# Kernel optimization log

Hardware: AMD Instinct MI355X
Metric: run time of the kernel (lower is better)

## Reference

```python
import jax, jax.numpy as jnp
import numpy as np

B = 32768                 # batch size (number of variants)
NUM_READ_FEATURES = 11
NUM_INFO_FEATURES = 9
PHI_DIMS = [NUM_READ_FEATURES, 64, 64]
OMEGA_DIMS = [NUM_INFO_FEATURES, 64, 64]
RHO_DIMS = [2 * 64 + 64, 128, 64, 1]
CAL_DIMS = [2, 5, 5, 1]


def _counts():
    # deterministic ragged group sizes in [5, 32], mean ~18.5, all nonempty
    return 5 + (np.arange(2 * B) % 28)


def _mlp_params(key, dims, prefix, out):
    for i, (din, dout) in enumerate(zip(dims[:-1], dims[1:])):
        key, k = jax.random.split(key)
        out[f"{prefix}_w{i}"] = (jax.random.normal(k, (din, dout), jnp.float32)
                                  / np.sqrt(din).astype(np.float32))
        out[f"{prefix}_b{i}"] = jnp.zeros((dout,), jnp.float32)
    return key


def _mlp(x, ws_bs):
    # Linear -> ReLU between layers, no activation after the last layer
    n = len(ws_bs) // 2
    for i in range(n):
        x = x @ ws_bs[2 * i] + ws_bs[2 * i + 1]
        if i < n - 1:
            x = jax.nn.relu(x)
    return x


def setup_inputs() -> dict:
    key = jax.random.key(0)
    counts = _counts()
    n_reads = int(counts.sum())  # 1,212,320
    key, k1, k2 = jax.random.split(key, 3)
    out = {
        "reads": jax.random.normal(k1, (n_reads, NUM_READ_FEATURES), jnp.float32),
        "info": jax.random.normal(k2, (B, NUM_INFO_FEATURES), jnp.float32),
        "end_indices": jnp.asarray(np.cumsum(counts), dtype=jnp.int64),
    }
    key = _mlp_params(key, PHI_DIMS, "phi", out)
    key = _mlp_params(key, OMEGA_DIMS, "omega", out)
    key = _mlp_params(key, RHO_DIMS, "rho", out)
    key = _mlp_params(key, CAL_DIMS, "cal", out)
    out["max_logit"] = jnp.asarray(10.0, jnp.float32)
    return out


def reference(reads, info, end_indices,
              phi_w0, phi_b0, phi_w1, phi_b1,
              omega_w0, omega_b0, omega_w1, omega_b1,
              rho_w0, rho_b0, rho_w1, rho_b1, rho_w2, rho_b2,
              cal_w0, cal_b0, cal_w1, cal_b1, cal_w2, cal_b2,
              max_logit):
    n_reads = reads.shape[0]
    num_seg = 2 * B
    # read r belongs to segment j where end_indices[j-1] <= r < end_indices[j]
    seg_ids = jnp.searchsorted(end_indices, jnp.arange(n_reads), side="right")

    phi_reads = jax.nn.sigmoid(_mlp(reads, [phi_w0, phi_b0, phi_w1, phi_b1]))  # [N, 64]
    weights = jnp.ones((n_reads, 1), phi_reads.dtype)  # weight_range == 0
    weighted = weights * phi_reads

    read_sums = jax.ops.segment_sum(weighted, seg_ids, num_segments=num_seg)      # [2B, 64]
    weight_sums = jax.ops.segment_sum(weights, seg_ids, num_segments=num_seg)     # [2B, 1]
    read_means = read_sums / weight_sums
    sq_weight_sums = jax.ops.segment_sum(jnp.square(weights), seg_ids, num_segments=num_seg)
    eff_counts = jnp.square(weight_sums) / sq_weight_sums                          # [2B, 1]

    ref_means, alt_means = read_means[:B], read_means[B:]
    eff_ref, eff_alt = eff_counts[:B], eff_counts[B:]

    omega_info = jax.nn.sigmoid(_mlp(info, [omega_w0, omega_b0, omega_w1, omega_b1]))
    concatenated = jnp.concatenate([ref_means, alt_means, omega_info], axis=1)     # [B, 192]
    logits = jnp.squeeze(_mlp(concatenated, [rho_w0, rho_b0, rho_w1, rho_b1, rho_w2, rho_b2]), -1)

    # Calibration: temperature from sqrt(alt_count), sqrt(ref_count)
    sqrt_counts = jnp.concatenate([jnp.sqrt(eff_alt), jnp.sqrt(eff_ref)], axis=1)  # [B, 2]
    temperatures = jnp.squeeze(_mlp(sqrt_counts, [cal_w0, cal_b0, cal_w1, cal_b1, cal_w2, cal_b2]), -1)
    calibrated = logits * temperatures
    return max_logit * jnp.tanh(calibrated / max_logit)
```

## Files before the change

### kernel.cpp

```cpp
#include <hip/hip_runtime.h>
#include <hip/hip_bf16.h>
#include <math.h>

#define NB 32768
#define NSEG 65536
#define NRF 11
#define NIF 9

typedef __attribute__((ext_vector_type(8))) short bf16x8;
typedef __attribute__((ext_vector_type(4))) float f32x4;

__device__ __forceinline__ short to_bf(float f) {
    __hip_bfloat16 h = __float2bfloat16(f);
    return *reinterpret_cast<short*>(&h);
}
__device__ __forceinline__ float bf2f(short s) {
    __hip_bfloat16 h = *reinterpret_cast<__hip_bfloat16*>(&s);
    return __bfloat162float(h);
}

__global__ __launch_bounds__(256) void k0_prep(
    const float* __restrict__ rw0, const float* __restrict__ rw1,
    const float* __restrict__ pw0, const float* __restrict__ pw1,
    short* __restrict__ w0th, short* __restrict__ w0tl,
    short* __restrict__ w1th, short* __restrict__ w1tl,
    short* __restrict__ p_w0t, short* __restrict__ p_w1t)
{
    const int idx = blockIdx.x * 256 + threadIdx.x;
    if (idx < 192 * 128) {
        const int k = idx >> 7, col = idx & 127;
        const float v = rw0[idx];
        const short hi = to_bf(v);
        const short lo = to_bf(v - bf2f(hi));
        w0th[col * 192 + k] = hi;
        w0tl[col * 192 + k] = lo;
    }
    if (idx < 128 * 64) {
        const int k = idx >> 6, col = idx & 63;
        const float v = rw1[idx];
        const short hi = to_bf(v);
        const short lo = to_bf(v - bf2f(hi));
        w1th[col * 128 + k] = hi;
        w1tl[col * 128 + k] = lo;
    }
    if (idx < 64 * 16) {
        const int col = idx >> 4, k = idx & 15;
        p_w0t[idx] = (k < NRF) ? to_bf(pw0[k * 64 + col]) : (short)0;
    }
    if (idx < 64 * 64) {
        const int col = idx >> 6, k = idx & 63;
        p_w1t[idx] = to_bf(pw1[k * 64 + col]);
    }
}

__global__ __launch_bounds__(256, 4) void k1_phi_mfma6(
    const float* __restrict__ reads,
    const int* __restrict__ endi,
    const short* __restrict__ p_w0t, const short* __restrict__ p_w1t,
    const float* __restrict__ b0, const float* __restrict__ b1,
    float* __restrict__ means)
{
    __shared__ short XA[256][24];
    __shared__ short HB[4][16][64];
    __shared__ int   smeta[9];

    const int tid  = threadIdx.x;
    const int lane = tid & 63;
    const int w    = tid >> 6;
    const int lg   = lane >> 4;
    const int lr   = lane & 15;
    const int k0   = lg * 8;
    const int s0   = blockIdx.x * 8;

    if (tid < 9) {
        const int s = s0 + tid - 1;
        smeta[tid] = (s < 0) ? 0 : endi[s];
    }
    __syncthreads();
    const int rb    = smeta[0];
    const int nrows = smeta[8] - rb;

    const int total = nrows * NRF;
    const float* __restrict__ rbase = reads + (size_t)rb * NRF;
    for (int i = tid; i < total; i += 256) {
        const int row = i / NRF;
        const int col = i - row * NRF;
        XA[row][col] = to_bf(rbase[i]);
    }
    for (int r = tid; r < nrows; r += 256) {
        XA[r][11] = 0;
        *(short4*)&XA[r][12] = (short4){0, 0, 0, 0};
    }
    __syncthreads();

    bf16x8 aW0[4];
#pragma unroll
    for (int nt = 0; nt < 4; ++nt) {
        bf16x8 z = {0, 0, 0, 0, 0, 0, 0, 0};
        if (lg < 2) z = *(const bf16x8*)&p_w0t[(nt * 16 + lr) * 16 + k0];
        aW0[nt] = z;
    }
    bf16x8 bW1[4][2];
#pragma unroll
    for (int nt = 0; nt < 4; ++nt)
#pragma unroll
        for (int ks = 0; ks < 2; ++ks)
            bW1[nt][ks] = *(const bf16x8*)&p_w1t[(nt * 16 + lr) * 64 + ks * 32 + k0];

    f32x4 cbias0[4];
#pragma unroll
    for (int nt = 0; nt < 4; ++nt)
#pragma unroll
        for (int q = 0; q < 4; ++q) cbias0[nt][q] = b0[nt * 16 + 4 * lg + q];
    f32x4 cbias1[4];
#pragma unroll
    for (int nt = 0; nt < 4; ++nt) {
        const float bv = b1[nt * 16 + lr];
#pragma unroll
        for (int q = 0; q < 4; ++q) cbias1[nt][q] = bv;
    }

    for (int q = 0; q < 2; ++q) {
        const int ls  = q * 4 + w;
        const int st  = smeta[ls] - rb;
        const int cnt = smeta[ls + 1] - smeta[ls];
        const int ntl = (cnt + 15) >> 4;
        float segsum[4] = {0.f, 0.f, 0.f, 0.f};

        for (int tt = 0; tt < ntl; ++tt) {
            int lrow = st + tt * 16 + lr;
            lrow = (lrow < nrows) ? lrow : (nrows - 1);
            bf16x8 xb = {0, 0, 0, 0, 0, 0, 0, 0};
            if (lg < 2) xb = *(const bf16x8*)&XA[lrow][k0];

            f32x4 d[4];
#pragma unroll
            for (int nt = 0; nt < 4; ++nt)
                d[nt] = __builtin_amdgcn_mfma_f32_16x16x32_bf16(aW0[nt], xb, cbias0[nt], 0, 0, 0);

#pragma unroll
            for (int nt = 0; nt < 4; ++nt) {
                short4 hp;
                hp.x = to_bf(fmaxf(d[nt][0], 0.f));
                hp.y = to_bf(fmaxf(d[nt][1], 0.f));
                hp.z = to_bf(fmaxf(d[nt][2], 0.f));
                hp.w = to_bf(fmaxf(d[nt][3], 0.f));
                const int blk = (2 * nt + (lg >> 1) + lr) & 7;
                *(short4*)&HB[w][lr][(blk << 3) + ((lg & 1) << 2)] = hp;
            }
            const bf16x8 h0 = *(const bf16x8*)&HB[w][lr][(((lg + lr) & 7) << 3)];
            const bf16x8 h1 = *(const bf16x8*)&HB[w][lr][(((4 + lg + lr) & 7) << 3)];
            f32x4 o[4];
#pragma unroll
            for (int nt = 0; nt < 4; ++nt) {
                f32x4 t = __builtin_amdgcn_mfma_f32_16x16x32_bf16(h0, bW1[nt][0], cbias1[nt], 0, 0, 0);
                o[nt]   = __builtin_amdgcn_mfma_f32_16x16x32_bf16(h1, bW1[nt][1], t, 0, 0, 0);
            }
            const int rowg = tt * 16 + 4 * lg;
#pragma unroll
            for (int nt = 0; nt < 4; ++nt) {
                float s = 0.f;
#pragma unroll
                for (int q2 = 0; q2 < 4; ++q2) {
                    const float p = __builtin_amdgcn_rcpf(1.f + __expf(-o[nt][q2]));
                    s += (rowg + q2 < cnt) ? p : 0.f;
                }
                segsum[nt] += s;
            }
        }
#pragma unroll
        for (int nt = 0; nt < 4; ++nt) {
            segsum[nt] += __shfl_xor(segsum[nt], 16);
            segsum[nt] += __shfl_xor(segsum[nt], 32);
        }
        if (lg == 0) {
            const float inv = 1.f / (float)cnt;
#pragma unroll
            for (int nt = 0; nt < 4; ++nt)
                means[(size_t)(s0 + ls) * 64 + nt * 16 + lr] = segsum[nt] * inv;
        }
    }
}

__global__ __launch_bounds__(256) void k2_omega(
    const float* __restrict__ info,
    const float* __restrict__ w0, const float* __restrict__ b0,
    const float* __restrict__ w1, const float* __restrict__ b1,
    float* __restrict__ om)
{
    __shared__ float hbuf[4][64];
    const int lane = threadIdx.x & 63;
    const int wid  = threadIdx.x >> 6;
    const int wg   = __builtin_amdgcn_readfirstlane((int)(blockIdx.x * 4 + wid));

    float w0c[NIF];
#pragma unroll
    for (int k = 0; k < NIF; ++k) w0c[k] = w0[k * 64 + lane];
    float w1c[64];
#pragma unroll
    for (int i = 0; i < 64; ++i) w1c[i] = w1[i * 64 + lane];
    const float b0l = b0[lane];
    const float b1l = b1[lane];

    for (int i = 0; i < 8; ++i) {
        const int b = wg * 8 + i;
        const float* __restrict__ x = info + (size_t)b * NIF;
        float h = b0l;
#pragma unroll
        for (int k = 0; k < NIF; ++k) h = fmaf(x[k], w0c[k], h);
        h = fmaxf(h, 0.f);
        hbuf[wid][lane] = h;
        float o = b1l;
        const float4* h4 = (const float4*)(&hbuf[wid][0]);
#pragma unroll
        for (int q = 0; q < 16; ++q) {
            float4 hv = h4[q];
            o = fmaf(hv.x, w1c[4 * q + 0], o);
            o = fmaf(hv.y, w1c[4 * q + 1], o);
            o = fmaf(hv.z, w1c[4 * q + 2], o);
            o = fmaf(hv.w, w1c[4 * q + 3], o);
        }
        om[(size_t)b * 64 + lane] = 1.f / (1.f + __expf(-o));
    }
}

__global__ __launch_bounds__(256) void k3_rho_mfma(
    const float* __restrict__ means, const float* __restrict__ om,
    const int* __restrict__ endi,
    const short* __restrict__ w0th, const short* __restrict__ w0tl,
    const short* __restrict__ w1th, const short* __restrict__ w1tl,
    const float* __restrict__ rb0, const float* __restrict__ rb1,
    const float* __restrict__ rw2, const float* __restrict__ rb2,
    const float* __restrict__ cw0, const float* __restrict__ cb0,
    const float* __restrict__ cw1, const float* __restrict__ cb1,
    const float* __restrict__ cw2, const float* __restrict__ cb2,
    const float* __restrict__ max_logit,
    float* __restrict__ out)
{
    __shared__ __align__(16) char smemA[18432];
    __shared__ __align__(16) char smemB[34816];
    short (*XH)[72]  = (short(*)[72])smemA;
    short (*XL)[72]  = (short(*)[72])(smemA + 9216);
    short (*HH)[136] = (short(*)[136])smemB;
    short (*HL)[136] = (short(*)[136])(smemB + 17408);
    float (*h2T)[68] = (float(*)[68])smemA;

    const int tid  = threadIdx.x;
    const int lane = tid & 63;
    const int w    = tid >> 6;
    const int lg   = lane >> 4;
    const int lr   = lane & 15;
    const int k0   = lg * 8;
    const int b0i  = blockIdx.x * 64;

    const int wbase = w * 32;
    float bias0[2];
#pragma unroll
    for (int nt = 0; nt < 2; ++nt) bias0[nt] = rb0[wbase + nt * 16 + lr];

    f32x4 acc[4][2];
#pragma unroll
    for (int rt = 0; rt < 4; ++rt)
#pragma unroll
        for (int nt = 0; nt < 2; ++nt) acc[rt][nt] = (f32x4){0.f, 0.f, 0.f, 0.f};

    for (int c = 0; c < 3; ++c) {
        const float* __restrict__ src =
            (c == 0) ? means + (size_t)b0i * 64 :
            (c == 1) ? means + (size_t)(NB + b0i) * 64 :
                       om    + (size_t)b0i * 64;
        __syncthreads();
        for (int idx = tid; idx < 64 * 64; idx += 256) {
            const int row = idx >> 6, col = idx & 63;
            const float v = src[(size_t)row * 64 + col];
            const short hi = to_bf(v);
            const short lo = to_bf(v - bf2f(hi));
            XH[row][col] = hi;
            XL[row][col] = lo;
        }
        __syncthreads();

#pragma unroll
        for (int ks = 0; ks < 2; ++ks) {
            const int koff = c * 64 + ks * 32 + k0;
            bf16x8 Bh[2], Bl[2];
#pragma unroll
            for (int nt = 0; nt < 2; ++nt) {
                const int col = wbase + nt * 16 + lr;
                Bh[nt] = *(const bf16x8*)&w0th[(size_t)col * 192 + koff];
                Bl[nt] = *(const bf16x8*)&w0tl[(size_t)col * 192 + koff];
            }
#pragma unroll
            for (int rt = 0; rt < 4; ++rt) {
                const bf16x8 Ah = *(const bf16x8*)&XH[rt * 16 + lr][ks * 32 + k0];
                const bf16x8 Al = *(const bf16x8*)&XL[rt * 16 + lr][ks * 32 + k0];
#pragma unroll
                for (int nt = 0; nt < 2; ++nt) {
                    acc[rt][nt] = __builtin_amdgcn_mfma_f32_16x16x32_bf16(Ah, Bh[nt], acc[rt][nt], 0, 0, 0);
                    acc[rt][nt] = __builtin_amdgcn_mfma_f32_16x16x32_bf16(Al, Bh[nt], acc[rt][nt], 0, 0, 0);
                    acc[rt][nt] = __builtin_amdgcn_mfma_f32_16x16x32_bf16(Ah, Bl[nt], acc[rt][nt], 0, 0, 0);
                }
            }
        }
    }
    __syncthreads();
#pragma unroll
    for (int rt = 0; rt < 4; ++rt)
#pragma unroll
        for (int nt = 0; nt < 2; ++nt)
#pragma unroll
            for (int r = 0; r < 4; ++r) {
                const int row = rt * 16 + 4 * lg + r;
                const int col = wbase + nt * 16 + lr;
                const float v = fmaxf(acc[rt][nt][r] + bias0[nt], 0.f);
                const short hi = to_bf(v);
                HH[row][col] = hi;
                HL[row][col] = to_bf(v - bf2f(hi));
            }
    __syncthreads();

    const int cbase = w * 16;
    const float bias1 = rb1[cbase + lr];
    f32x4 acc2[4];
#pragma unroll
    for (int rt = 0; rt < 4; ++rt) acc2[rt] = (f32x4){0.f, 0.f, 0.f, 0.f};

#pragma unroll
    for (int ks = 0; ks < 4; ++ks) {
        const int koff = ks * 32 + k0;
        const int col  = cbase + lr;
        const bf16x8 Bh = *(const bf16x8*)&w1th[(size_t)col * 128 + koff];
        const bf16x8 Bl = *(const bf16x8*)&w1tl[(size_t)col * 128 + koff];
#pragma unroll
        for (int rt = 0; rt < 4; ++rt) {
            const bf16x8 Ah = *(const bf16x8*)&HH[rt * 16 + lr][koff];
            const bf16x8 Al = *(const bf16x8*)&HL[rt * 16 + lr][koff];
            acc2[rt] = __builtin_amdgcn_mfma_f32_16x16x32_bf16(Ah, Bh, acc2[rt], 0, 0, 0);
            acc2[rt] = __builtin_amdgcn_mfma_f32_16x16x32_bf16(Al, Bh, acc2[rt], 0, 0, 0);
            acc2[rt] = __builtin_amdgcn_mfma_f32_16x16x32_bf16(Ah, Bl, acc2[rt], 0, 0, 0);
        }
    }
#pragma unroll
    for (int rt = 0; rt < 4; ++rt)
#pragma unroll
        for (int r = 0; r < 4; ++r)
            h2T[cbase + lr][rt * 16 + 4 * lg + r] = fmaxf(acc2[rt][r] + bias1, 0.f);
    __syncthreads();

    if (w == 0) {
        const int b = b0i + lane;
        float l0 = rb2[0], l1 = 0.f, l2 = 0.f, l3 = 0.f;
#pragma unroll
        for (int j = 0; j < 16; ++j) {
            l0 = fmaf(h2T[j][lane],      rw2[j],      l0);
            l1 = fmaf(h2T[16 + j][lane], rw2[16 + j], l1);
            l2 = fmaf(h2T[32 + j][lane], rw2[32 + j], l2);
            l3 = fmaf(h2T[48 + j][lane], rw2[48 + j], l3);
        }
        const float logit = (l0 + l1) + (l2 + l3);

        const int er1 = endi[b];
        const int er0 = (b == 0) ? 0 : endi[b - 1];
        const int ea1 = endi[NB + b];
        const int ea0 = endi[NB + b - 1];
        const float x0 = sqrtf((float)(ea1 - ea0));
        const float x1 = sqrtf((float)(er1 - er0));

        float t5[5];
#pragma unroll
        for (int m = 0; m < 5; ++m)
            t5[m] = fmaxf(cb0[m] + x0 * cw0[m] + x1 * cw0[5 + m], 0.f);
        float t5b[5];
#pragma unroll
        for (int m = 0; m < 5; ++m) {
            float v = cb1[m];
#pragma unroll
            for (int i = 0; i < 5; ++i) v = fmaf(t5[i], cw1[i * 5 + m], v);
            t5b[m] = fmaxf(v, 0.f);
        }
        float temp = cb2[0];
#pragma unroll
        for (int m = 0; m < 5; ++m) temp = fmaf(t5b[m], cw2[m], temp);

        const float ml = max_logit[0];
        out[b] = ml * tanhf((logit * temp) / ml);
    }
}

extern "C" void kernel_launch(void* const* d_in, const int* in_sizes, int n_in,
                              void* d_out, int out_size, void* d_ws, size_t ws_size,
                              hipStream_t stream)
{
    const float* reads  = (const float*)d_in[0];
    const float* info   = (const float*)d_in[1];
    const int*   endi   = (const int*)d_in[2];
    const float* phi_w0 = (const float*)d_in[3];
    const float* phi_b0 = (const float*)d_in[4];
    const float* phi_w1 = (const float*)d_in[5];
    const float* phi_b1 = (const float*)d_in[6];
    const float* om_w0  = (const float*)d_in[7];
    const float* om_b0  = (const float*)d_in[8];
    const float* om_w1  = (const float*)d_in[9];
    const float* om_b1  = (const float*)d_in[10];
    const float* rw0    = (const float*)d_in[11];
    const float* rb0    = (const float*)d_in[12];
    const float* rw1    = (const float*)d_in[13];
    const float* rb1    = (const float*)d_in[14];
    const float* rw2    = (const float*)d_in[15];
    const float* rb2    = (const float*)d_in[16];
    const float* cw0    = (const float*)d_in[17];
    const float* cb0    = (const float*)d_in[18];
    const float* cw1    = (const float*)d_in[19];
    const float* cb1    = (const float*)d_in[20];
    const float* cw2    = (const float*)d_in[21];
    const float* cb2    = (const float*)d_in[22];
    const float* mlog   = (const float*)d_in[23];

    char* ws = (char*)d_ws;
    float* means = (float*)ws;
    float* om    = (float*)(ws + 16777216);
    short* w0th  = (short*)(ws + 25165824);
    short* w0tl  = (short*)(ws + 25165824 + 49152);
    short* w1th  = (short*)(ws + 25165824 + 98304);
    short* w1tl  = (short*)(ws + 25165824 + 114688);
    short* p_w0t = (short*)(ws + 25165824 + 131072);
    short* p_w1t = (short*)(ws + 25165824 + 133120);
    float* out   = (float*)d_out;

    hipLaunchKernelGGL(k0_prep, dim3(96), dim3(256), 0, stream,
                       rw0, rw1, phi_w0, phi_w1,
                       w0th, w0tl, w1th, w1tl, p_w0t, p_w1t);
    hipLaunchKernelGGL(k1_phi_mfma6, dim3(8192), dim3(256), 0, stream,
                       reads, endi, p_w0t, p_w1t, phi_b0, phi_b1, means);
    hipLaunchKernelGGL(k2_omega, dim3(1024), dim3(256), 0, stream,
                       info, om_w0, om_b0, om_w1, om_b1, om);
    hipLaunchKernelGGL(k3_rho_mfma, dim3(512), dim3(256), 0, stream,
                       means, om, endi, w0th, w0tl, w1th, w1tl,
                       rb0, rb1, rw2, rb2,
                       cw0, cb0, cw1, cb1, cw2, cb2, mlog, out);
}
```

Before: 102.6 us.

## Keep phi hidden layer in registers by permuting W1 K-order, dropping LDS round-trip

```diff
diff --git a/kernel.cpp b/kernel.cpp
--- a/kernel.cpp
+++ b/kernel.cpp
@@ -9,6 +9,7 @@
 
 typedef __attribute__((ext_vector_type(8))) short bf16x8;
 typedef __attribute__((ext_vector_type(4))) float f32x4;
+typedef __attribute__((ext_vector_type(4))) unsigned u32x4;
 
 __device__ __forceinline__ short to_bf(float f) {
     __hip_bfloat16 h = __float2bfloat16(f);
@@ -17,6 +18,11 @@
 __device__ __forceinline__ float bf2f(short s) {
     __hip_bfloat16 h = *reinterpret_cast<__hip_bfloat16*>(&s);
     return __bfloat162float(h);
+}
+__device__ __forceinline__ unsigned cvt_pk_bf16(float lo, float hi) {
+    unsigned r;
+    asm("v_cvt_pk_bf16_f32 %0, %1, %2" : "=v"(r) : "v"(lo), "v"(hi));
+    return r;
 }
 
 __global__ __launch_bounds__(256) void k0_prep(
@@ -48,12 +54,15 @@
         p_w0t[idx] = (k < NRF) ? to_bf(pw0[k * 64 + col]) : (short)0;
     }
     if (idx < 64 * 64) {
-        const int col = idx >> 6, k = idx & 63;
+        const int col = idx >> 6, kp = idx & 63;
+        const int c = kp >> 5, rem = kp & 31;
+        const int lgi = rem >> 3, e = rem & 7;
+        const int k = 32 * c + 16 * (e >> 2) + 4 * lgi + (e & 3);
         p_w1t[idx] = to_bf(pw1[k * 64 + col]);
     }
 }
 
-__global__ __launch_bounds__(256, 4) void k1_phi_mfma6(
+__global__ __launch_bounds__(256, 4) void k1_phi_mfma9(
     const float* __restrict__ reads,
     const int* __restrict__ endi,
     const short* __restrict__ p_w0t, const short* __restrict__ p_w1t,
@@ -61,7 +70,6 @@
     float* __restrict__ means)
 {
     __shared__ short XA[256][24];
-    __shared__ short HB[4][16][64];
     __shared__ int   smeta[9];
 
     const int tid  = threadIdx.x;
@@ -138,34 +146,37 @@
             for (int nt = 0; nt < 4; ++nt)
                 d[nt] = __builtin_amdgcn_mfma_f32_16x16x32_bf16(aW0[nt], xb, cbias0[nt], 0, 0, 0);
 
+            float h[4][4];
+#pragma unroll
+            for (int nt = 0; nt < 4; ++nt)
+#pragma unroll
+                for (int q2 = 0; q2 < 4; ++q2) h[nt][q2] = fmaxf(d[nt][q2], 0.f);
+            union { u32x4 u; bf16x8 s; } a2c0, a2c1;
+            a2c0.u = (u32x4){ cvt_pk_bf16(h[0][0], h[0][1]),
+                              cvt_pk_bf16(h[0][2], h[0][3]),
+                              cvt_pk_bf16(h[1][0], h[1][1]),
+                              cvt_pk_bf16(h[1][2], h[1][3]) };
+            a2c1.u = (u32x4){ cvt_pk_bf16(h[2][0], h[2][1]),
+                              cvt_pk_bf16(h[2][2], h[2][3]),
+                              cvt_pk_bf16(h[3][0], h[3][1]),
+                              cvt_pk_bf16(h[3][2], h[3][3]) };
+
+            f32x4 o[4];
 #pragma unroll
             for (int nt = 0; nt < 4; ++nt) {
-                short4 hp;
-                hp.x = to_bf(fmaxf(d[nt][0], 0.f));
-                hp.y = to_bf(fmaxf(d[nt][1], 0.f));
-                hp.z = to_bf(fmaxf(d[nt][2], 0.f));
-                hp.w = to_bf(fmaxf(d[nt][3], 0.f));
-                const int blk = (2 * nt + (lg >> 1) + lr) & 7;
-                *(short4*)&HB[w][lr][(blk << 3) + ((lg & 1) << 2)] = hp;
-            }
-            const bf16x8 h0 = *(const bf16x8*)&HB[w][lr][(((lg + lr) & 7) << 3)];
-            const bf16x8 h1 = *(const bf16x8*)&HB[w][lr][(((4 + lg + lr) & 7) << 3)];
-            f32x4 o[4];
-#pragma unroll
-            for (int nt = 0; nt < 4; ++nt) {
-                f32x4 t = __builtin_amdgcn_mfma_f32_16x16x32_bf16(h0, bW1[nt][0], cbias1[nt], 0, 0, 0);
-                o[nt]   = __builtin_amdgcn_mfma_f32_16x16x32_bf16(h1, bW1[nt][1], t, 0, 0, 0);
+                f32x4 t = __builtin_amdgcn_mfma_f32_16x16x32_bf16(a2c0.s, bW1[nt][0], cbias1[nt], 0, 0, 0);
+                o[nt]   = __builtin_amdgcn_mfma_f32_16x16x32_bf16(a2c1.s, bW1[nt][1], t, 0, 0, 0);
             }
             const int rowg = tt * 16 + 4 * lg;
 #pragma unroll
             for (int nt = 0; nt < 4; ++nt) {
-                float s = 0.f;
+                float s = segsum[nt];
 #pragma unroll
                 for (int q2 = 0; q2 < 4; ++q2) {
                     const float p = __builtin_amdgcn_rcpf(1.f + __expf(-o[nt][q2]));
                     s += (rowg + q2 < cnt) ? p : 0.f;
                 }
-                segsum[nt] += s;
+                segsum[nt] = s;
             }
         }
 #pragma unroll
@@ -430,7 +441,7 @@
     hipLaunchKernelGGL(k0_prep, dim3(96), dim3(256), 0, stream,
                        rw0, rw1, phi_w0, phi_w1,
                        w0th, w0tl, w1th, w1tl, p_w0t, p_w1t);
-    hipLaunchKernelGGL(k1_phi_mfma6, dim3(8192), dim3(256), 0, stream,
+    hipLaunchKernelGGL(k1_phi_mfma9, dim3(8192), dim3(256), 0, stream,
                        reads, endi, p_w0t, p_w1t, phi_b0, phi_b1, means);
     hipLaunchKernelGGL(k2_omega, dim3(1024), dim3(256), 0, stream,
                        info, om_w0, om_b0, om_w1, om_b1, om);
```

After: 101.1 us. No clear change (-1.5%).
